# Kernel optimization log

Hardware: AMD Instinct MI355X
Metric: run time of the kernel (lower is better)

Reference implementation:

```python
import jax, jax.numpy as jnp
import numpy as np

N, K, C_IN, C = 64, 64, 128, 128


def setup_inputs() -> dict:
    key = jax.random.key(0)
    ks = jax.random.split(key, 12)
    s_in = 1.0 / np.sqrt(C_IN + 1)
    s_c = 1.0 / np.sqrt(C)
    s_2c = 1.0 / np.sqrt(2 * C)
    return {
        "t": jax.random.uniform(ks[0], (1,), dtype=jnp.float32),
        "x": jax.random.normal(ks[1], (N, K, C_IN), dtype=jnp.float32),
        # ConcatLinear: Linear(C_IN + 1, C) applied to cat([x, t], -1)
        "W_lin": jax.random.normal(ks[2], (C, C_IN + 1), dtype=jnp.float32) * s_in,
        "b_lin": jax.random.normal(ks[3], (C,), dtype=jnp.float32) * s_in,
        # unary_passing: Linear(C,C) -> tanh -> Linear(C,C)
        "Wu1": jax.random.normal(ks[4], (C, C), dtype=jnp.float32) * s_c,
        "bu1": jax.random.normal(ks[5], (C,), dtype=jnp.float32) * s_c,
        "Wu2": jax.random.normal(ks[6], (C, C), dtype=jnp.float32) * s_c,
        "bu2": jax.random.normal(ks[7], (C,), dtype=jnp.float32) * s_c,
        # binary_passing: Linear(2C,C) -> tanh -> Linear(C,C)
        "Wb1": jax.random.normal(ks[8], (C, 2 * C), dtype=jnp.float32) * s_2c,
        "bb1": jax.random.normal(ks[9], (C,), dtype=jnp.float32) * s_2c,
        "Wb2": jax.random.normal(ks[10], (C, C), dtype=jnp.float32) * s_c,
        "bb2": jax.random.normal(ks[11], (C,), dtype=jnp.float32) * s_c,
    }


def reference(t, x, W_lin, b_lin, Wu1, bu1, Wu2, bu2, Wb1, bb1, Wb2, bb2):
    n, k, _ = x.shape
    # linear_map: ConcatLinear(t, x) = Linear(cat([x, t*ones], -1))
    tt = jnp.broadcast_to(t.reshape(1, 1, 1), (n, k, 1)).astype(x.dtype)
    h = jnp.concatenate([x, tt], axis=-1) @ W_lin.T + b_lin  # [N,K,C]

    # unary message
    unary = jnp.tanh(h @ Wu1.T + bu1) @ Wu2.T + bu2  # [N,K,C]

    # binary message. h_matrix[n,i,j] = cat([h[n,j], h[n,i]]); split Wb1 into
    # the halves acting on each part to avoid materializing the 2C concat.
    A = h @ Wb1[:, :C].T          # contribution of h[n,j], [N,K,C]
    B = h @ Wb1[:, C:].T          # contribution of h[n,i], [N,K,C]
    pre = A[:, None, :, :] + B[:, :, None, :] + bb1       # [N,i,j,C]
    msg = jnp.tanh(pre) @ Wb2.T + bb2                     # [N,i,j,C]

    # fully-connected graph: E[i,j] = 1 - eye (E is None, masks is None)
    E = 1.0 - jnp.eye(k, dtype=x.dtype)                   # [i,j]
    msg = msg * E[None, :, :, None]
    denom = 1.0 + jnp.sum(E, axis=0)                      # per-j, [K]
    binary = jnp.sum(msg, axis=1) / denom[None, :, None]  # [N,K,C]

    return unary + binary
```

## Files before the change

kernel.cpp:

```cpp
#include <hip/hip_runtime.h>

#define LS 132
#define USTR 20
#define ROW_ELEMS 524288
#define EXPC 2.8853900817779268f

__device__ __forceinline__ float tanh_fast(float x) {
    float e = __builtin_amdgcn_exp2f(x * EXPC);
    return 1.0f - 2.0f * __builtin_amdgcn_rcpf(e + 1.0f);
}

__device__ __forceinline__ void stage64(const float* __restrict__ X, int r0,
                                        float* __restrict__ xs, int tid) {
    const float4* src = reinterpret_cast<const float4*>(X + (size_t)r0 * 128);
#pragma unroll
    for (int p = 0; p < 8; ++p) {
        const int q = p * 256 + tid;
        const int r = q >> 5;
        const int k4 = (q & 31) << 2;
        *reinterpret_cast<float4*>(&xs[r * LS + k4]) = src[q];
    }
}

template <int NC>
__device__ __forceinline__ void accum_lds(const float* __restrict__ xs,
                                          const float* __restrict__ wt,
                                          int lane, int wc0,
                                          float (&acc)[NC]) {
#pragma unroll 8
    for (int kq = 0; kq < 32; ++kq) {
        const float4 a =
            *reinterpret_cast<const float4*>(&xs[lane * LS + kq * 4]);
#pragma unroll
        for (int c = 0; c < NC; ++c) {
            const float4 w = *reinterpret_cast<const float4*>(
                &wt[(wc0 + c) * 128 + kq * 4]);
            acc[c] = fmaf(a.x, w.x, acc[c]);
            acc[c] = fmaf(a.y, w.y, acc[c]);
            acc[c] = fmaf(a.z, w.z, acc[c]);
            acc[c] = fmaf(a.w, w.w, acc[c]);
        }
    }
}

__global__ __launch_bounds__(256) void k1_h(const float* __restrict__ x,
                                            const float* __restrict__ W_lin,
                                            const float* __restrict__ b_lin,
                                            const float* __restrict__ tp,
                                            float* __restrict__ h) {
    __shared__ float xs[64 * LS];
    __shared__ float wt[8 * 128];
    const int tid = threadIdx.x;
    const int lane = tid & 63;
    const int wv = __builtin_amdgcn_readfirstlane(tid >> 6);
    const int r0 = blockIdx.x * 64;
    const int cb = blockIdx.y * 8;
    stage64(x, r0, xs, tid);
#pragma unroll
    for (int p = 0; p < 4; ++p) {
        const int q = p * 256 + tid;
        const int row = q >> 7;
        const int col = q & 127;
        wt[row * 128 + col] = W_lin[(cb + row) * 129 + col];
    }
    __syncthreads();
    float acc[2] = {0.f, 0.f};
    accum_lds<2>(xs, wt, lane, wv * 2, acc);
    const int c0 = cb + wv * 2;
    const float tv = tp[0];
    float2 o;
    o.x = acc[0] + b_lin[c0 + 0] + tv * W_lin[(c0 + 0) * 129 + 128];
    o.y = acc[1] + b_lin[c0 + 1] + tv * W_lin[(c0 + 1) * 129 + 128];
    *reinterpret_cast<float2*>(&h[(size_t)(r0 + lane) * 128 + c0]) = o;
}

__global__ __launch_bounds__(256) void k2_fused(
    const float* __restrict__ h, const float* __restrict__ Wu1,
    const float* __restrict__ bu1, const float* __restrict__ Wb1,
    const float* __restrict__ bb1, float* __restrict__ T,
    float* __restrict__ S) {
    __shared__ float smem[64 * LS + 32 * 128];
    float* xs = smem;
    float* wt = smem + 64 * LS;
    float* us = smem;
    float* vs = smem + 64 * USTR;
    const int tid = threadIdx.x;
    const int lane = tid & 63;
    const int wv = __builtin_amdgcn_readfirstlane(tid >> 6);
    const int r0 = blockIdx.x * 64;
    const int j = blockIdx.y;
    stage64(h, r0, xs, tid);
    {
        const int cb = j < 8 ? j * 16 : 0;
        const int cg0 = j >= 8 ? (j - 8) * 32 : 0;
#pragma unroll
        for (int p = 0; p < 4; ++p) {
            const int q = p * 256 + tid;
            const int row = q >> 5;
            const int k4 = (q & 31) << 2;
            const float* src;
            if (j < 8)
                src = (row < 16) ? (Wb1 + (cb + row) * 256 + k4)
                                 : (Wb1 + (cb + row - 16) * 256 + 128 + k4);
            else
                src = Wu1 + (cg0 + row) * 128 + k4;
            *reinterpret_cast<float4*>(&wt[row * 128 + k4]) =
                *reinterpret_cast<const float4*>(src);
        }
    }
    __syncthreads();

    if (j < 8) {
        const int cb = j * 16;
        const bool isB = wv >= 2;
        const int half = wv & 1;
        const int c0 = cb + half * 8;
        const int wc0 = (isB ? 16 : 0) + half * 8;
        float acc[8] = {0.f, 0.f, 0.f, 0.f, 0.f, 0.f, 0.f, 0.f};
        accum_lds<8>(xs, wt, lane, wc0, acc);
        float e[8];
#pragma unroll
        for (int c = 0; c < 8; ++c) {
            const float v = isB ? (acc[c] + bb1[c0 + c]) : acc[c];
            e[c] = __builtin_amdgcn_exp2f(v * EXPC);
        }
        __syncthreads();
        float* dstl = (isB ? vs : us) + lane * USTR + half * 8;
        *reinterpret_cast<float4*>(dstl) = make_float4(e[0], e[1], e[2], e[3]);
        *reinterpret_cast<float4*>(dstl + 4) =
            make_float4(e[4], e[5], e[6], e[7]);
        __syncthreads();

        const int lc = wv * 4;
        const float4 u =
            *reinterpret_cast<const float4*>(&us[lane * USTR + lc]);
        float s0 = 0.f, s1 = 0.f, s2 = 0.f, s3 = 0.f;
#pragma unroll 8
        for (int i = 0; i < 64; ++i) {
            const float4 v =
                *reinterpret_cast<const float4*>(&vs[i * USTR + lc]);
            s0 += __builtin_amdgcn_rcpf(fmaf(u.x, v.x, 1.0f));
            s1 += __builtin_amdgcn_rcpf(fmaf(u.y, v.y, 1.0f));
            s2 += __builtin_amdgcn_rcpf(fmaf(u.z, v.z, 1.0f));
            s3 += __builtin_amdgcn_rcpf(fmaf(u.w, v.w, 1.0f));
        }
        const float4 vj =
            *reinterpret_cast<const float4*>(&vs[lane * USTR + lc]);
        float4 o;
        o.x = (63.0f - 2.0f * (s0 - __builtin_amdgcn_rcpf(fmaf(u.x, vj.x, 1.0f)))) * 0.015625f;
        o.y = (63.0f - 2.0f * (s1 - __builtin_amdgcn_rcpf(fmaf(u.y, vj.y, 1.0f)))) * 0.015625f;
        o.z = (63.0f - 2.0f * (s2 - __builtin_amdgcn_rcpf(fmaf(u.z, vj.z, 1.0f)))) * 0.015625f;
        o.w = (63.0f - 2.0f * (s3 - __builtin_amdgcn_rcpf(fmaf(u.w, vj.w, 1.0f)))) * 0.015625f;
        *reinterpret_cast<float4*>(&S[(size_t)(r0 + lane) * 128 + cb + lc]) = o;
    } else {
        const int c0 = (j - 8) * 32 + wv * 8;
        float acc[8] = {0.f, 0.f, 0.f, 0.f, 0.f, 0.f, 0.f, 0.f};
        accum_lds<8>(xs, wt, lane, wv * 8, acc);
        float4 v0, v1;
        v0.x = tanh_fast(acc[0] + bu1[c0 + 0]);
        v0.y = tanh_fast(acc[1] + bu1[c0 + 1]);
        v0.z = tanh_fast(acc[2] + bu1[c0 + 2]);
        v0.w = tanh_fast(acc[3] + bu1[c0 + 3]);
        v1.x = tanh_fast(acc[4] + bu1[c0 + 4]);
        v1.y = tanh_fast(acc[5] + bu1[c0 + 5]);
        v1.z = tanh_fast(acc[6] + bu1[c0 + 6]);
        v1.w = tanh_fast(acc[7] + bu1[c0 + 7]);
        float* dst = T + (size_t)(r0 + lane) * 128 + c0;
        *reinterpret_cast<float4*>(dst) = v0;
        *reinterpret_cast<float4*>(dst + 4) = v1;
    }
}

__global__ __launch_bounds__(256) void k4_out(
    const float* __restrict__ T, const float* __restrict__ S,
    const float* __restrict__ Wu2, const float* __restrict__ Wb2,
    const float* __restrict__ bu2, const float* __restrict__ bb2,
    float* __restrict__ out) {
    __shared__ float xs[64 * LS];
    __shared__ float wt[8 * 128];
    const int tid = threadIdx.x;
    const int lane = tid & 63;
    const int wv = __builtin_amdgcn_readfirstlane(tid >> 6);
    const int r0 = blockIdx.x * 64;
    const int cb = blockIdx.y * 8;
    stage64(T, r0, xs, tid);
    {
        const int row = tid >> 5;
        const int k4 = (tid & 31) << 2;
        *reinterpret_cast<float4*>(&wt[row * 128 + k4]) =
            *reinterpret_cast<const float4*>(Wu2 + (cb + row) * 128 + k4);
    }
    __syncthreads();
    float acc[2] = {0.f, 0.f};
    accum_lds<2>(xs, wt, lane, wv * 2, acc);
    __syncthreads();
    stage64(S, r0, xs, tid);
    {
        const int row = tid >> 5;
        const int k4 = (tid & 31) << 2;
        *reinterpret_cast<float4*>(&wt[row * 128 + k4]) =
            *reinterpret_cast<const float4*>(Wb2 + (cb + row) * 128 + k4);
    }
    __syncthreads();
    accum_lds<2>(xs, wt, lane, wv * 2, acc);
    const int c0 = cb + wv * 2;
    float2 o;
    o.x = acc[0] + bu2[c0 + 0] + 0.984375f * bb2[c0 + 0];
    o.y = acc[1] + bu2[c0 + 1] + 0.984375f * bb2[c0 + 1];
    *reinterpret_cast<float2*>(&out[(size_t)(r0 + lane) * 128 + c0]) = o;
}

extern "C" void kernel_launch(void* const* d_in, const int* in_sizes, int n_in,
                              void* d_out, int out_size, void* d_ws,
                              size_t ws_size, hipStream_t stream) {
    const float* t = (const float*)d_in[0];
    const float* x = (const float*)d_in[1];
    const float* W_lin = (const float*)d_in[2];
    const float* b_lin = (const float*)d_in[3];
    const float* Wu1 = (const float*)d_in[4];
    const float* bu1 = (const float*)d_in[5];
    const float* Wu2 = (const float*)d_in[6];
    const float* bu2 = (const float*)d_in[7];
    const float* Wb1 = (const float*)d_in[8];
    const float* bb1 = (const float*)d_in[9];
    const float* Wb2 = (const float*)d_in[10];
    const float* bb2 = (const float*)d_in[11];
    float* out = (float*)d_out;

    float* ws = (float*)d_ws;
    float* h = ws;
    float* T = ws + 1 * ROW_ELEMS;
    float* S = ws + 2 * ROW_ELEMS;

    k1_h<<<dim3(64, 16), 256, 0, stream>>>(x, W_lin, b_lin, t, h);
    k2_fused<<<dim3(64, 12), 256, 0, stream>>>(h, Wu1, bu1, Wb1, bb1, T, S);
    k4_out<<<dim3(64, 16), 256, 0, stream>>>(T, S, Wu2, Wb2, bu2, bb2, out);
    (void)in_sizes; (void)n_in; (void)out_size; (void)ws_size;
}
```

Measured before the change: 37.37 us.

## Read weights via wave-uniform scalar loads instead of LDS staging in k1/k4

The per-wave weight rows in k1_h and k4_out are now read straight from global memory with wave-uniform addresses, which lets the compiler issue scalar loads, instead of first staging them in shared memory. k4_out now stages T and S into separate LDS buffers together behind a single barrier. Each wave computes 4 output columns instead of 2, which halves the k4 grid and widens the output store to float4. This removes LDS weight traffic and barriers, in exchange for higher LDS use per block in k4 (lower occupancy) and reliance on the scalar cache for the weights.

```diff
diff --git a/kernel.cpp b/kernel.cpp
--- a/kernel.cpp
+++ b/kernel.cpp
@@ -43,30 +43,42 @@
     }
 }
 
+template <int NC>
+__device__ __forceinline__ void accum_sload(const float* __restrict__ xs,
+                                            int lane,
+                                            const float* const (&wrow)[NC],
+                                            float (&acc)[NC]) {
+#pragma unroll 8
+    for (int kq = 0; kq < 32; ++kq) {
+        const float4 a =
+            *reinterpret_cast<const float4*>(&xs[lane * LS + kq * 4]);
+#pragma unroll
+        for (int c = 0; c < NC; ++c) {
+            const float* w = wrow[c] + kq * 4;
+            acc[c] = fmaf(a.x, w[0], acc[c]);
+            acc[c] = fmaf(a.y, w[1], acc[c]);
+            acc[c] = fmaf(a.z, w[2], acc[c]);
+            acc[c] = fmaf(a.w, w[3], acc[c]);
+        }
+    }
+}
+
 __global__ __launch_bounds__(256) void k1_h(const float* __restrict__ x,
                                             const float* __restrict__ W_lin,
                                             const float* __restrict__ b_lin,
                                             const float* __restrict__ tp,
                                             float* __restrict__ h) {
     __shared__ float xs[64 * LS];
-    __shared__ float wt[8 * 128];
     const int tid = threadIdx.x;
     const int lane = tid & 63;
     const int wv = __builtin_amdgcn_readfirstlane(tid >> 6);
     const int r0 = blockIdx.x * 64;
-    const int cb = blockIdx.y * 8;
+    const int c0 = blockIdx.y * 8 + wv * 2;
     stage64(x, r0, xs, tid);
-#pragma unroll
-    for (int p = 0; p < 4; ++p) {
-        const int q = p * 256 + tid;
-        const int row = q >> 7;
-        const int col = q & 127;
-        wt[row * 128 + col] = W_lin[(cb + row) * 129 + col];
-    }
     __syncthreads();
     float acc[2] = {0.f, 0.f};
-    accum_lds<2>(xs, wt, lane, wv * 2, acc);
-    const int c0 = cb + wv * 2;
+    const float* wrow[2] = {W_lin + (c0 + 0) * 129, W_lin + (c0 + 1) * 129};
+    accum_sload<2>(xs, lane, wrow, acc);
     const float tv = tp[0];
     float2 o;
     o.x = acc[0] + b_lin[c0 + 0] + tv * W_lin[(c0 + 0) * 129 + 128];
@@ -176,38 +188,33 @@
     const float* __restrict__ Wu2, const float* __restrict__ Wb2,
     const float* __restrict__ bu2, const float* __restrict__ bb2,
     float* __restrict__ out) {
-    __shared__ float xs[64 * LS];
-    __shared__ float wt[8 * 128];
+    __shared__ float xsT[64 * LS];
+    __shared__ float xsS[64 * LS];
     const int tid = threadIdx.x;
     const int lane = tid & 63;
     const int wv = __builtin_amdgcn_readfirstlane(tid >> 6);
     const int r0 = blockIdx.x * 64;
-    const int cb = blockIdx.y * 8;
-    stage64(T, r0, xs, tid);
+    const int c0 = blockIdx.y * 16 + wv * 4;
+    stage64(T, r0, xsT, tid);
+    stage64(S, r0, xsS, tid);
+    __syncthreads();
+    float acc[4] = {0.f, 0.f, 0.f, 0.f};
     {
-        const int row = tid >> 5;
-        const int k4 = (tid & 31) << 2;
-        *reinterpret_cast<float4*>(&wt[row * 128 + k4]) =
-            *reinterpret_cast<const float4*>(Wu2 + (cb + row) * 128 + k4);
-    }
-    __syncthreads();
-    float acc[2] = {0.f, 0.f};
-    accum_lds<2>(xs, wt, lane, wv * 2, acc);
-    __syncthreads();
-    stage64(S, r0, xs, tid);
+        const float* wrow[4] = {Wu2 + (c0 + 0) * 128, Wu2 + (c0 + 1) * 128,
+                                Wu2 + (c0 + 2) * 128, Wu2 + (c0 + 3) * 128};
+        accum_sload<4>(xsT, lane, wrow, acc);
+    }
     {
-        const int row = tid >> 5;
-        const int k4 = (tid & 31) << 2;
-        *reinterpret_cast<float4*>(&wt[row * 128 + k4]) =
-            *reinterpret_cast<const float4*>(Wb2 + (cb + row) * 128 + k4);
-    }
-    __syncthreads();
-    accum_lds<2>(xs, wt, lane, wv * 2, acc);
-    const int c0 = cb + wv * 2;
-    float2 o;
+        const float* wrow[4] = {Wb2 + (c0 + 0) * 128, Wb2 + (c0 + 1) * 128,
+                                Wb2 + (c0 + 2) * 128, Wb2 + (c0 + 3) * 128};
+        accum_sload<4>(xsS, lane, wrow, acc);
+    }
+    float4 o;
     o.x = acc[0] + bu2[c0 + 0] + 0.984375f * bb2[c0 + 0];
     o.y = acc[1] + bu2[c0 + 1] + 0.984375f * bb2[c0 + 1];
-    *reinterpret_cast<float2*>(&out[(size_t)(r0 + lane) * 128 + c0]) = o;
+    o.z = acc[2] + bu2[c0 + 2] + 0.984375f * bb2[c0 + 2];
+    o.w = acc[3] + bu2[c0 + 3] + 0.984375f * bb2[c0 + 3];
+    *reinterpret_cast<float4*>(&out[(size_t)(r0 + lane) * 128 + c0]) = o;
 }
 
 extern "C" void kernel_launch(void* const* d_in, const int* in_sizes, int n_in,
@@ -234,6 +241,6 @@
 
     k1_h<<<dim3(64, 16), 256, 0, stream>>>(x, W_lin, b_lin, t, h);
     k2_fused<<<dim3(64, 12), 256, 0, stream>>>(h, Wu1, bu1, Wb1, bb1, T, S);
-    k4_out<<<dim3(64, 16), 256, 0, stream>>>(T, S, Wu2, Wb2, bu2, bb2, out);
+    k4_out<<<dim3(64, 8), 256, 0, stream>>>(T, S, Wu2, Wb2, bu2, bb2, out);
     (void)in_sizes; (void)n_in; (void)out_size; (void)ws_size;
 }
```

Result: no change. 36.83 us (-1.4%).
